# Optimization experiments

Hardware: AMD Instinct MI355X
Metric: run time of the kernel (lower is better)

Reference implementation:

```python
import jax, jax.numpy as jnp
import numpy as np

DIM = 768
NUM_HEADS = 12
HEAD_DIM = DIM // NUM_HEADS
SCALE = HEAD_DIM ** -0.5


def setup_inputs() -> dict:
    key = jax.random.key(0)
    ks = jax.random.split(key, 12)
    B, N, C, H = 8, 1024, DIM, NUM_HEADS
    s = 0.02
    return {
        'q_in': jax.random.normal(ks[0], (B, N, C), jnp.float32),
        'kv_in': jax.random.normal(ks[1], (B, N, C), jnp.float32),
        'Wq': jax.random.normal(ks[2], (C, C), jnp.float32) * s,
        'Wk': jax.random.normal(ks[3], (C, C), jnp.float32) * s,
        'Wv': jax.random.normal(ks[4], (C, C), jnp.float32) * s,
        'Wp': jax.random.normal(ks[5], (C, C), jnp.float32) * s,
        'bp': jnp.zeros((C,), jnp.float32),
        'W_dy2': jax.random.normal(ks[6], (H, C), jnp.float32) * s,  # lf gate linear (out=H)
        'b_dy2': jnp.zeros((H,), jnp.float32),
        'W_dy': jax.random.normal(ks[7], (H, C), jnp.float32) * s,   # hf gate linear
        'b_dy': jnp.zeros((H,), jnp.float32),
        'lf_gamma': jnp.full((C,), 1e-5, jnp.float32),
        'hf_gamma': jnp.full((C,), 1e-5, jnp.float32),
        'star_scale': jnp.ones((1,), jnp.float32),
        'star_bias': jnp.zeros((1,), jnp.float32),
    }


def reference(q_in, kv_in, Wq, Wk, Wv, Wp, bp, W_dy2, b_dy2, W_dy, b_dy,
              lf_gamma, hf_gamma, star_scale, star_bias):
    B, Nq, C = q_in.shape
    Nk = kv_in.shape[1]
    H, D = NUM_HEADS, HEAD_DIM

    # StarReLU on query tokens (ignore_cls_token = 0)
    dy_feat = star_scale * jnp.square(jax.nn.relu(q_in)) + star_bias  # (B,Nq,C)

    # low-freq dynamic gate: tanh(linear) per head, repeated over head_dim
    dy_lf = jnp.tanh(jnp.einsum('bnc,hc->bnh', dy_feat, W_dy2) + b_dy2)  # (B,Nq,H)
    dy_lf = jnp.repeat(dy_lf, D, axis=-1)  # (B,Nq,C)

    # high-freq dynamic gate: rational-of-softplus^2
    dy = jax.nn.softplus(jnp.einsum('bnc,hc->bnh', dy_feat, W_dy) + b_dy)
    dy2 = jnp.square(dy)
    dy_hf = 2.0 * dy2 / (dy2 + 0.3678)
    dy_hf = jnp.repeat(dy_hf, D, axis=-1)  # (B,Nq,C)

    # projections (torch Linear: y = x @ W.T), split heads
    q = jnp.einsum('bnc,dc->bnd', q_in, Wq).reshape(B, Nq, H, D).transpose(0, 2, 1, 3)
    k = jnp.einsum('bnc,dc->bnd', kv_in, Wk).reshape(B, Nk, H, D).transpose(0, 2, 1, 3)
    v = jnp.einsum('bnc,dc->bnd', kv_in, Wv).reshape(B, Nk, H, D).transpose(0, 2, 1, 3)

    attn = jnp.einsum('bhqd,bhkd->bhqk', q * SCALE, k)
    attn = jax.nn.softmax(attn, axis=-1)
    x_attn = jnp.einsum('bhqk,bhkd->bhqd', attn, v)
    x_attn = x_attn.transpose(0, 2, 1, 3).reshape(B, Nq, C)

    # Nk == Nq branch: per-token residual high-frequency component
    v_reshape = v.transpose(0, 2, 1, 3).reshape(B, Nk, C)
    v_hf = v_reshape - x_attn

    x_attn = x_attn + x_attn * dy_lf * lf_gamma
    x_attn = x_attn + dy_hf * v_hf * hf_gamma

    out = jnp.einsum('bnc,dc->bnd', x_attn, Wp) + bp
    return out
```

## Files before the change

### kernel.cpp

```cpp
#include <hip/hip_runtime.h>
#include <hip/hip_bf16.h>
#include <stdint.h>

typedef unsigned short u16;
typedef unsigned int u32;
typedef unsigned long long u64;
typedef __attribute__((ext_vector_type(8))) short short8;
typedef __attribute__((ext_vector_type(4))) float f32x4;

#define LOG2E 1.44269504f

static __device__ __forceinline__ u16 f2bf(float f) {
    u32 x = __float_as_uint(f);
    u32 r = (x + 0x7FFFu + ((x >> 16) & 1u)) >> 16;
    return (u16)r;
}
static __device__ __forceinline__ float bf2f(u16 u) {
    return __uint_as_float(((u32)u) << 16);
}
static __device__ __forceinline__ u32 pk2(float lo, float hi) {
    __hip_bfloat162 t = __float22bfloat162_rn(float2{lo, hi});
    union { __hip_bfloat162 b; u32 u; } cv;
    cv.b = t;
    return cv.u;
}
static __device__ __forceinline__ float fexp2(float x) {
#if __has_builtin(__builtin_amdgcn_exp2f)
    return __builtin_amdgcn_exp2f(x);
#else
    return exp2f(x);
#endif
}

static __device__ __forceinline__ void g2l16(const void* g, void* l) {
    __builtin_amdgcn_global_load_lds((const __attribute__((address_space(1))) void*)g,
                                     (__attribute__((address_space(3))) void*)l, 16, 0, 0);
}

__global__ __launch_bounds__(256) void k_cvt_all(
    const float* __restrict__ q_in, const float* __restrict__ kv_in,
    const float* __restrict__ Wq, const float* __restrict__ Wk,
    const float* __restrict__ Wv, const float* __restrict__ Wp,
    const float* __restrict__ Wdy2, const float* __restrict__ Wdy,
    u16* __restrict__ qbf, u16* __restrict__ kvbf, u16* __restrict__ Wqb,
    u16* __restrict__ Wkb, u16* __restrict__ Wvb, u16* __restrict__ Wpb,
    u16* __restrict__ wgb) {
    int i = blockIdx.x * 256 + threadIdx.x;
    const float* src;
    u16* dst;
    int so, dofs;
    if (i < 786432) { src = q_in; dst = qbf; so = i; dofs = i; }
    else if (i < 1572864) { src = kv_in; dst = kvbf; so = i - 786432; dofs = so; }
    else if (i < 1646592) { src = Wq; dst = Wqb; so = i - 1572864; dofs = so; }
    else if (i < 1720320) { src = Wk; dst = Wkb; so = i - 1646592; dofs = so; }
    else if (i < 1794048) { src = Wv; dst = Wvb; so = i - 1720320; dofs = so; }
    else if (i < 1867776) { src = Wp; dst = Wpb; so = i - 1794048; dofs = so; }
    else if (i < 1870080) {
        int e = i - 1867776;
        dst = wgb; dofs = e;
        if (e < 1152) { src = Wdy2; so = e; }
        else { src = Wdy; so = e - 1152; }
    } else return;
    const float4* p = (const float4*)src + (size_t)so * 2;
    float4 a = p[0], b = p[1];
    short8 o;
    o[0] = f2bf(a.x); o[1] = f2bf(a.y); o[2] = f2bf(a.z); o[3] = f2bf(a.w);
    o[4] = f2bf(b.x); o[5] = f2bf(b.y); o[6] = f2bf(b.z); o[7] = f2bf(b.w);
    *((short8*)dst + dofs) = o;
}

__global__ __launch_bounds__(64) void k_gates(
    const u16* __restrict__ qbf, const u16* __restrict__ wgb,
    const float* __restrict__ bdy2, const float* __restrict__ bdy,
    const float* __restrict__ star_s, const float* __restrict__ star_b,
    float* __restrict__ glf, float* __restrict__ ghf) {
    int lane = threadIdx.x;
    int g = lane >> 4, c = lane & 15;
    int row0 = blockIdx.x * 16;
    float ss = star_s[0], sb = star_b[0];
    f32x4 acc[2];
    acc[0] = (f32x4){0.f, 0.f, 0.f, 0.f};
    acc[1] = (f32x4){0.f, 0.f, 0.f, 0.f};
    for (int t = 0; t < 24; ++t) {
        int k0 = t * 32;
        short8 x8 = *(const short8*)(qbf + (size_t)(row0 + c) * 768 + k0 + g * 8);
        float f[8];
#pragma unroll
        for (int j = 0; j < 8; ++j) {
            float x = fmaxf(bf2f((u16)x8[j]), 0.f);
            f[j] = ss * x * x + sb;
        }
        union { u32 u[4]; short8 s8; } au;
#pragma unroll
        for (int j = 0; j < 4; ++j) au.u[j] = pk2(f[2 * j], f[2 * j + 1]);
        short8 b0 = *(const short8*)(wgb + (size_t)c * 768 + k0 + g * 8);
        short8 b1 = (short8){0, 0, 0, 0, 0, 0, 0, 0};
        if (c < 8)
            b1 = *(const short8*)(wgb + (size_t)(16 + c) * 768 + k0 + g * 8);
        acc[0] = __builtin_amdgcn_mfma_f32_16x16x32_bf16(au.s8, b0, acc[0], 0, 0, 0);
        acc[1] = __builtin_amdgcn_mfma_f32_16x16x32_bf16(au.s8, b1, acc[1], 0, 0, 0);
    }
#pragma unroll
    for (int n = 0; n < 2; ++n)
#pragma unroll
        for (int r = 0; r < 4; ++r) {
            int token = row0 + g * 4 + r;
            int o = n * 16 + c;
            float v = acc[n][r];
            if (o < 12) {
                glf[(size_t)token * 12 + o] = tanhf(v + bdy2[o]);
            } else if (o < 24) {
                float x = v + bdy[o - 12];
                float sp = (x > 15.f) ? x : log1pf(expf(x));
                float d2 = sp * sp;
                ghf[(size_t)token * 12 + (o - 12)] = 2.f * d2 / (d2 + 0.3678f);
            }
        }
}

__device__ __forceinline__ void gemm_core(const u16* __restrict__ A,
                                          const u16* __restrict__ W, u16* As,
                                          u16* Bs, int rowA0, int rowB0,
                                          int lane, int w, int wm, int wn,
                                          f32x4 acc[4][4]) {
    int g = lane >> 4, c = lane & 15;
#pragma unroll
    for (int m = 0; m < 4; ++m)
#pragma unroll
        for (int n = 0; n < 4; ++n) acc[m][n] = (f32x4){0.f, 0.f, 0.f, 0.f};

    auto stage = [&](int buf, int k0) {
#pragma unroll
        for (int j = 0; j < 2; ++j) {
            int L = w * 128 + j * 64 + lane;
            int p = L >> 3, s8 = L & 7;
            int t2 = s8 ^ (p & 7);
            int row = 2 * p + (t2 >> 2);
            int chunk = t2 & 3;
            size_t go = (size_t)row * 768 + k0 + chunk * 8;
            g2l16(A + (size_t)rowA0 * 768 + go, As + buf * 4096 + L * 8);
            g2l16(W + (size_t)rowB0 * 768 + go, Bs + buf * 4096 + L * 8);
        }
    };

    stage(0, 0);
    stage(1, 32);
    int cur = 0, nxt = 2;
    for (int t = 0; t < 24; ++t) {
        if (t < 23) asm volatile("s_waitcnt vmcnt(4)" ::: "memory");
        else        asm volatile("s_waitcnt vmcnt(0)" ::: "memory");
        __builtin_amdgcn_s_barrier();
        if (t < 22) stage(nxt, (t + 2) * 32);
        short8 a[4], b[4];
#pragma unroll
        for (int m = 0; m < 4; ++m) {
            int row = wm * 64 + m * 16 + c;
            int off = (row >> 1) * 64 +
                      ((((row & 1) << 2) | g) ^ ((row >> 1) & 7)) * 8;
            a[m] = *(const short8*)(As + cur * 4096 + off);
        }
#pragma unroll
        for (int n = 0; n < 4; ++n) {
            int row = wn * 64 + n * 16 + c;
            int off = (row >> 1) * 64 +
                      ((((row & 1) << 2) | g) ^ ((row >> 1) & 7)) * 8;
            b[n] = *(const short8*)(Bs + cur * 4096 + off);
        }
        __builtin_amdgcn_s_setprio(1);
#pragma unroll
        for (int m = 0; m < 4; ++m)
#pragma unroll
            for (int n = 0; n < 4; ++n)
                acc[m][n] = __builtin_amdgcn_mfma_f32_16x16x32_bf16(
                    a[m], b[n], acc[m][n], 0, 0, 0);
        __builtin_amdgcn_s_setprio(0);
        cur = (cur == 2) ? 0 : cur + 1;
        nxt = (nxt == 2) ? 0 : nxt + 1;
    }
}

static __device__ __forceinline__ int park_wb(int row, int col) {
    return row * 256 + ((col * 2) ^ (((row >> 2) & 3) << 5));
}
static __device__ __forceinline__ int park_rb(int srow, int sch) {
    return srow * 256 + ((sch * 16) ^ (((srow >> 2) & 3) << 5));
}

__global__ __launch_bounds__(256, 3) void k_gemm_qkv(
    const u16* __restrict__ qbf, const u16* __restrict__ kvbf,
    const u16* __restrict__ Wqb, const u16* __restrict__ Wkb,
    const u16* __restrict__ Wvb, u16* __restrict__ Qb, u16* __restrict__ Kb,
    u16* __restrict__ VTg, u16* __restrict__ vlin) {
    __shared__ __align__(16) u16 smem[24576];
    u16* As = smem;
    u16* Bs = smem + 12288;
    int bid = blockIdx.x;
    int logical = (bid & 7) * 144 + (bid >> 3);
    int panel = logical / 18, sub = logical % 18;
    int type = sub / 6, tn = sub % 6;
    int tid = threadIdx.x, lane = tid & 63, w = tid >> 6;
    int g = lane >> 4, c = lane & 15;
    int wm = w >> 1, wn = w & 1;
    int rowA0 = panel * 128, rowB0 = tn * 128;
    const u16* A = (type == 0) ? qbf : kvbf;
    const u16* W = (type == 0) ? Wqb : (type == 1) ? Wkb : Wvb;

    f32x4 acc[4][4];
    gemm_core(A, W, As, Bs, rowA0, rowB0, lane, w, wm, wn, acc);
    __syncthreads();

    if (type < 2) {
        u16* dst = (type == 0) ? Qb : Kb;
        const float scl = (type == 0) ? (0.125f * LOG2E) : 1.0f;
#pragma unroll
        for (int m = 0; m < 4; ++m)
#pragma unroll
            for (int n = 0; n < 4; ++n)
#pragma unroll
                for (int r = 0; r < 4; ++r) {
                    int row = wm * 64 + m * 16 + g * 4 + r;
                    int col = wn * 64 + n * 16 + c;
                    *(u16*)((char*)smem + park_wb(row, col)) =
                        f2bf(acc[m][n][r] * scl);
                }
        __syncthreads();
#pragma unroll
        for (int j = 0; j < 8; ++j) {
            int idx = j * 256 + tid;
            int srow = idx >> 4, sch = idx & 15;
            short8 v = *(const short8*)((char*)smem + park_rb(srow, sch));
            int token = rowA0 + srow;
            int col0 = rowB0 + sch * 8;
            int bb = token >> 10, nn = token & 1023, hh = col0 >> 6,
                dd = col0 & 63;
            *(short8*)(dst + ((size_t)(bb * 12 + hh) << 16) + (nn << 6) + dd) = v;
        }
    } else {
#pragma unroll
        for (int m = 0; m < 4; ++m)
#pragma unroll
            for (int n = 0; n < 4; ++n)
#pragma unroll
                for (int r = 0; r < 4; ++r) {
                    int row = wm * 64 + m * 16 + g * 4 + r;
                    int col = wn * 64 + n * 16 + c;
                    *(u16*)((char*)smem + park_wb(row, col)) = f2bf(acc[m][n][r]);
                }
        __syncthreads();
#pragma unroll
        for (int j = 0; j < 8; ++j) {
            int idx = j * 256 + tid;
            int srow = idx >> 4, sch = idx & 15;
            short8 v = *(const short8*)((char*)smem + park_rb(srow, sch));
            *(short8*)(vlin + (size_t)(rowA0 + srow) * 768 + rowB0 + sch * 8) = v;
        }
        __syncthreads();
#pragma unroll
        for (int m = 0; m < 4; ++m)
#pragma unroll
            for (int n = 0; n < 4; ++n)
#pragma unroll
                for (int r = 0; r < 4; ++r) {
                    int rl = wm * 64 + m * 16 + g * 4 + r;
                    int cl = wn * 64 + n * 16 + c;
                    smem[cl * 128 + rl] = f2bf(acc[m][n][r]);
                }
        __syncthreads();
        int bb = rowA0 >> 10, nn0 = rowA0 & 1023;
#pragma unroll
        for (int j = 0; j < 8; ++j) {
            int idx = j * 256 + tid;
            int rT = idx >> 4, cc = idx & 15;
            int dout = rowB0 + rT, hh = dout >> 6, dd = dout & 63;
            const u16* srow = smem + rT * 128 + cc * 8;
            size_t robase = ((size_t)(bb * 12 + hh) * 64 + dd) * 1024;
#pragma unroll
            for (int e2 = 0; e2 < 4; ++e2) {
                int n0 = nn0 + cc * 8 + 2 * e2;
                int t6 = n0 & 63;
                int pos = (((t6 >> 1) & 1) << 5) | (((t6 >> 2) & 3) << 3) |
                          (((t6 >> 4) & 3) << 1) | (t6 & 1);
                u32 val = (u32)srow[2 * e2] | ((u32)srow[2 * e2 + 1] << 16);
                *(u32*)(VTg + robase + (n0 & ~63) + pos) = val;
            }
        }
    }
}

__global__ __launch_bounds__(256, 3) void k_gemm_out(
    const u16* __restrict__ xf, const u16* __restrict__ Wpb,
    const float* __restrict__ bp, float* __restrict__ out) {
    __shared__ __align__(16) u16 smem[24576];
    u16* As = smem;
    u16* Bs = smem + 12288;
    int bid = blockIdx.x;
    int logical = (bid & 7) * 48 + (bid >> 3);
    int c48 = logical % 48;
    int tm = (logical / 48) * 8 + c48 / 6, tn = c48 % 6;
    int tid = threadIdx.x, lane = tid & 63, w = tid >> 6;
    int g = lane >> 4, c = lane & 15;
    int wm = w >> 1, wn = w & 1;
    int rowA0 = tm * 128, rowB0 = tn * 128;

    f32x4 acc[4][4];
    gemm_core(xf, Wpb, As, Bs, rowA0, rowB0, lane, w, wm, wn, acc);

    float bias[4];
#pragma unroll
    for (int n = 0; n < 4; ++n) bias[n] = bp[rowB0 + wn * 64 + n * 16 + c];

    char* F = (char*)smem;
#pragma unroll
    for (int p = 0; p < 2; ++p) {
        __syncthreads();
        if (wm == p) {
#pragma unroll
            for (int m = 0; m < 4; ++m)
#pragma unroll
                for (int n = 0; n < 4; ++n)
#pragma unroll
                    for (int r = 0; r < 4; ++r) {
                        int lrow = m * 16 + g * 4 + r;
                        int col = wn * 64 + n * 16 + c;
                        int byte = lrow * 512 +
                                   ((col * 4) ^ (((lrow >> 2) & 3) << 6));
                        *(float*)(F + byte) = acc[m][n][r] + bias[n];
                    }
        }
        __syncthreads();
#pragma unroll
        for (int j = 0; j < 8; ++j) {
            int idx = j * 256 + tid;
            int srow = idx >> 5, sch = idx & 31;
            int byte = srow * 512 + ((sch * 16) ^ (((srow >> 2) & 3) << 6));
            float4 v = *(const float4*)(F + byte);
            *(float4*)(out + (size_t)(rowA0 + p * 64 + srow) * 768 + rowB0 +
                       sch * 4) = v;
        }
    }
}

__global__ __launch_bounds__(256, 3) void k_attn(
    const u16* __restrict__ Qb, const u16* __restrict__ Kb,
    const u16* __restrict__ VTg, const u16* __restrict__ vlin,
    const float* __restrict__ glf, const float* __restrict__ ghf,
    const float* __restrict__ lfg, const float* __restrict__ hfg,
    u16* __restrict__ xfinal) {
    __shared__ __align__(16) u16 Ks[12288];
    __shared__ __align__(16) u16 Vs[12288];
    int b8 = blockIdx.x;
    int sw = (b8 & 7) * 96 + (b8 >> 3);
    int bh = sw >> 3, qblk = sw & 7;
    int bb = bh / 12, hh = bh % 12;
    int tid = threadIdx.x, lane = tid & 63, w = tid >> 6;
    int g = lane >> 4, c = lane & 15;
    const char* Kp = (const char*)(Kb + ((size_t)bh << 16));
    const char* Vp = (const char*)(VTg + ((size_t)bh << 16));
    const u16* Qp = Qb + ((size_t)bh << 16);
    int q0 = qblk * 128 + w * 32;

    short8 qf[2][2];
#pragma unroll
    for (int qb = 0; qb < 2; ++qb)
#pragma unroll
        for (int ks = 0; ks < 2; ++ks)
            qf[qb][ks] = *(const short8*)(Qp + (size_t)(q0 + qb * 16 + c) * 64 +
                                          ks * 32 + g * 8);

    f32x4 o[2][4];
#pragma unroll
    for (int qb = 0; qb < 2; ++qb)
#pragma unroll
        for (int n = 0; n < 4; ++n) o[qb][n] = (f32x4){0.f, 0.f, 0.f, 0.f};
    f32x4 o5[2];
    o5[0] = (f32x4){0.f, 0.f, 0.f, 0.f};
    o5[1] = (f32x4){0.f, 0.f, 0.f, 0.f};
    const short8 vones = (short8){(short)0x3F80, (short)0x3F80, (short)0x3F80,
                                  (short)0x3F80, (short)0x3F80, (short)0x3F80,
                                  (short)0x3F80, (short)0x3F80};

    int kgo[2], vgo[2], ldo[2];
#pragma unroll
    for (int h = 0; h < 2; ++h) {
        int idx = w * 64 + lane + h * 256;
        int row = idx >> 3;
        int colb = ((idx & 7) * 16) ^ ((row & 7) << 4);
        kgo[h] = row * 128 + colb;
        vgo[h] = row * 2048 + colb;
        ldo[h] = (w * 64 + h * 256) * 16;
    }

    auto stage = [&](int bi, int t) {
#pragma unroll
        for (int h = 0; h < 2; ++h) {
            g2l16(Kp + (size_t)t * 8192 + kgo[h], (char*)Ks + bi * 8192 + ldo[h]);
            g2l16(Vp + (size_t)t * 128 + vgo[h], (char*)Vs + bi * 8192 + ldo[h]);
        }
    };

    stage(0, 0);
    stage(1, 1);
    int cur = 0, nxt = 2;
    int cs = (c & 7) << 4;
    for (int t = 0; t < 16; ++t) {
        if (t < 15) asm volatile("s_waitcnt vmcnt(4)" ::: "memory");
        else        asm volatile("s_waitcnt vmcnt(0)" ::: "memory");
        __builtin_amdgcn_s_barrier();
        if (t < 14) stage(nxt, t + 2);
        const char* Kbase = (const char*)Ks + cur * 8192;
        const char* Vbase = (const char*)Vs + cur * 8192;
        short8 kf[4][2], vf[4][2];
#pragma unroll
        for (int m = 0; m < 4; ++m) {
            int rowb = (m * 16 + c) * 128;
#pragma unroll
            for (int ks = 0; ks < 2; ++ks)
                kf[m][ks] = *(const short8*)(Kbase + rowb +
                                             ((g * 16 + ks * 64) ^ cs));
        }
#pragma unroll
        for (int n = 0; n < 4; ++n) {
            int rowb = (n * 16 + c) * 128;
#pragma unroll
            for (int a = 0; a < 2; ++a)
                vf[n][a] = *(const short8*)(Vbase + rowb +
                                            ((a * 64 + g * 16) ^ cs));
        }
#pragma unroll
        for (int qb = 0; qb < 2; ++qb) {
            f32x4 s[4];
            __builtin_amdgcn_s_setprio(1);
#pragma unroll
            for (int m = 0; m < 4; ++m) {
                s[m] = __builtin_amdgcn_mfma_f32_16x16x32_bf16(
                    kf[m][0], qf[qb][0], (f32x4){0.f, 0.f, 0.f, 0.f}, 0, 0, 0);
                s[m] = __builtin_amdgcn_mfma_f32_16x16x32_bf16(
                    kf[m][1], qf[qb][1], s[m], 0, 0, 0);
            }
            __builtin_amdgcn_s_setprio(0);
            u32 P2[4][2];
#pragma unroll
            for (int m = 0; m < 4; ++m) {
#pragma unroll
                for (int r = 0; r < 4; ++r) s[m][r] = fexp2(s[m][r]);
                P2[m][0] = pk2(s[m][0], s[m][1]);
                P2[m][1] = pk2(s[m][2], s[m][3]);
            }
#pragma unroll
            for (int a = 0; a < 2; ++a) {
                union { u32 u[4]; short8 s8; } pu;
                pu.u[0] = P2[0][a]; pu.u[1] = P2[1][a];
                pu.u[2] = P2[2][a]; pu.u[3] = P2[3][a];
                __builtin_amdgcn_s_setprio(1);
#pragma unroll
                for (int n = 0; n < 4; ++n)
                    o[qb][n] = __builtin_amdgcn_mfma_f32_16x16x32_bf16(
                        pu.s8, vf[n][a], o[qb][n], 0, 0, 0);
                o5[qb] = __builtin_amdgcn_mfma_f32_16x16x32_bf16(
                    pu.s8, vones, o5[qb], 0, 0, 0);
                __builtin_amdgcn_s_setprio(0);
            }
        }
        cur = (cur == 2) ? 0 : cur + 1;
        nxt = (nxt == 2) ? 0 : nxt + 1;
    }
    __syncthreads();

    u16* X = &Ks[0];
#pragma unroll
    for (int qb = 0; qb < 2; ++qb) {
        float rl[4];
#pragma unroll
        for (int r = 0; r < 4; ++r) rl[r] = 1.0f / o5[qb][r];
#pragma unroll
        for (int n = 0; n < 4; ++n)
#pragma unroll
            for (int r = 0; r < 4; ++r) {
                int row = w * 32 + qb * 16 + 4 * g + r;
                int col = n * 16 + c;
                int byte = row * 128 + ((col * 2) ^ ((row & 3) << 4));
                *(u16*)((char*)X + byte) = f2bf(o[qb][n][r] * rl[r]);
            }
    }
    __syncthreads();
    {
        int row = tid >> 1, half = tid & 1;
        size_t token = (size_t)bb * 1024 + qblk * 128 + row;
        float alf = glf[token * 12 + hh];
        float ahf = ghf[token * 12 + hh];
        int dbase = hh * 64 + half * 32;
        const u16* vbase = vlin + token * 768 + dbase;
        u16* obase = xfinal + token * 768 + dbase;
#pragma unroll
        for (int j = 0; j < 4; ++j) {
            int phys = ((half * 4 + j) ^ (row & 3)) * 16;
            short8 xa8 = *(const short8*)((char*)X + row * 128 + phys);
            short8 vl8 = *(const short8*)(vbase + j * 8);
            float4 lg0 = *(const float4*)(lfg + dbase + j * 8);
            float4 lg1 = *(const float4*)(lfg + dbase + j * 8 + 4);
            float4 hg0 = *(const float4*)(hfg + dbase + j * 8);
            float4 hg1 = *(const float4*)(hfg + dbase + j * 8 + 4);
            float lg[8] = {lg0.x, lg0.y, lg0.z, lg0.w, lg1.x, lg1.y, lg1.z, lg1.w};
            float hg[8] = {hg0.x, hg0.y, hg0.z, hg0.w, hg1.x, hg1.y, hg1.z, hg1.w};
            short8 oo;
#pragma unroll
            for (int e = 0; e < 8; ++e) {
                float xa = bf2f((u16)xa8[e]);
                float v = bf2f((u16)vl8[e]);
                float val = xa + xa * alf * lg[e] + ahf * (v - xa) * hg[e];
                oo[e] = f2bf(val);
            }
            *(short8*)(obase + j * 8) = oo;
        }
    }
}

extern "C" void kernel_launch(void* const* d_in, const int* in_sizes, int n_in,
                              void* d_out, int out_size, void* d_ws,
                              size_t ws_size, hipStream_t stream) {
    const float* q_in = (const float*)d_in[0];
    const float* kv_in = (const float*)d_in[1];
    const float* Wq = (const float*)d_in[2];
    const float* Wk = (const float*)d_in[3];
    const float* Wv = (const float*)d_in[4];
    const float* Wp = (const float*)d_in[5];
    const float* bp = (const float*)d_in[6];
    const float* Wdy2 = (const float*)d_in[7];
    const float* bdy2 = (const float*)d_in[8];
    const float* Wdy = (const float*)d_in[9];
    const float* bdy = (const float*)d_in[10];
    const float* lfg = (const float*)d_in[11];
    const float* hfg = (const float*)d_in[12];
    const float* st_s = (const float*)d_in[13];
    const float* st_b = (const float*)d_in[14];
    float* out = (float*)d_out;

    char* ws = (char*)d_ws;
    const size_t MC2 = (size_t)8192 * 768 * 2;
    const size_t WB = (size_t)768 * 768 * 2;
    u16* qbf = (u16*)(ws);
    u16* kvbf = (u16*)(ws + MC2);
    u16* Wqb = (u16*)(ws + 2 * MC2);
    u16* Wkb = (u16*)(ws + 2 * MC2 + WB);
    u16* Wvb = (u16*)(ws + 2 * MC2 + 2 * WB);
    u16* Wpb = (u16*)(ws + 2 * MC2 + 3 * WB);
    u16* Qb = (u16*)(ws + 2 * MC2 + 4 * WB);
    u16* Kb = (u16*)(ws + 3 * MC2 + 4 * WB);
    u16* VTg = (u16*)(ws + 4 * MC2 + 4 * WB);
    u16* vlin = (u16*)(ws + 5 * MC2 + 4 * WB);
    float* glf = (float*)(ws + 6 * MC2 + 4 * WB);
    float* ghf = (float*)(ws + 6 * MC2 + 4 * WB + (size_t)8192 * 12 * 4);
    u16* wgb = (u16*)(ws + 6 * MC2 + 4 * WB + (size_t)8192 * 12 * 8);
    u16* xfinal = qbf;

    k_cvt_all<<<7305, 256, 0, stream>>>(q_in, kv_in, Wq, Wk, Wv, Wp, Wdy2,
                                        Wdy, qbf, kvbf, Wqb, Wkb, Wvb, Wpb,
                                        wgb);
    k_gates<<<512, 64, 0, stream>>>(qbf, wgb, bdy2, bdy, st_s, st_b, glf, ghf);
    k_gemm_qkv<<<1152, 256, 0, stream>>>(qbf, kvbf, Wqb, Wkb, Wvb, Qb, Kb,
                                         VTg, vlin);
    k_attn<<<768, 256, 0, stream>>>(Qb, Kb, VTg, vlin, glf, ghf, lfg, hfg,
                                    xfinal);
    k_gemm_out<<<384, 256, 0, stream>>>(xfinal, Wpb, bp, out);
}
```

Before: 133.7 us.

## Fuse activation fp32-to-bf16 conversion into QKV GEMM and drop attention LDS staging

Stops pre-converting q_in and kv_in to bf16 in a separate pass. The QKV GEMM now loads fp32 A tiles into registers and converts and writes them to LDS itself, and the gates kernel reads fp32 directly. This removes a full activation read and write pass over global memory. Separately, the attention kernel now reads K and V fragments straight from global memory instead of through triple-buffered LDS, freeing shared memory so occupancy can rise to 4 blocks per SM; this risks uncoalesced, redundant global loads and exposed latency.

Result: slower. 244.7 us (+83.0%).

```diff
diff --git a/kernel.cpp b/kernel.cpp
--- a/kernel.cpp
+++ b/kernel.cpp
@@ -37,26 +37,22 @@
                                      (__attribute__((address_space(3))) void*)l, 16, 0, 0);
 }
 
-__global__ __launch_bounds__(256) void k_cvt_all(
-    const float* __restrict__ q_in, const float* __restrict__ kv_in,
+__global__ __launch_bounds__(256) void k_cvt_w(
     const float* __restrict__ Wq, const float* __restrict__ Wk,
     const float* __restrict__ Wv, const float* __restrict__ Wp,
     const float* __restrict__ Wdy2, const float* __restrict__ Wdy,
-    u16* __restrict__ qbf, u16* __restrict__ kvbf, u16* __restrict__ Wqb,
-    u16* __restrict__ Wkb, u16* __restrict__ Wvb, u16* __restrict__ Wpb,
-    u16* __restrict__ wgb) {
+    u16* __restrict__ Wqb, u16* __restrict__ Wkb, u16* __restrict__ Wvb,
+    u16* __restrict__ Wpb, u16* __restrict__ wgb) {
     int i = blockIdx.x * 256 + threadIdx.x;
     const float* src;
     u16* dst;
     int so, dofs;
-    if (i < 786432) { src = q_in; dst = qbf; so = i; dofs = i; }
-    else if (i < 1572864) { src = kv_in; dst = kvbf; so = i - 786432; dofs = so; }
-    else if (i < 1646592) { src = Wq; dst = Wqb; so = i - 1572864; dofs = so; }
-    else if (i < 1720320) { src = Wk; dst = Wkb; so = i - 1646592; dofs = so; }
-    else if (i < 1794048) { src = Wv; dst = Wvb; so = i - 1720320; dofs = so; }
-    else if (i < 1867776) { src = Wp; dst = Wpb; so = i - 1794048; dofs = so; }
-    else if (i < 1870080) {
-        int e = i - 1867776;
+    if (i < 73728) { src = Wq; dst = Wqb; so = i; dofs = so; }
+    else if (i < 147456) { src = Wk; dst = Wkb; so = i - 73728; dofs = so; }
+    else if (i < 221184) { src = Wv; dst = Wvb; so = i - 147456; dofs = so; }
+    else if (i < 294912) { src = Wp; dst = Wpb; so = i - 221184; dofs = so; }
+    else if (i < 297216) {
+        int e = i - 294912;
         dst = wgb; dofs = e;
         if (e < 1152) { src = Wdy2; so = e; }
         else { src = Wdy; so = e - 1152; }
@@ -70,7 +66,7 @@
 }
 
 __global__ __launch_bounds__(64) void k_gates(
-    const u16* __restrict__ qbf, const u16* __restrict__ wgb,
+    const float* __restrict__ qin, const u16* __restrict__ wgb,
     const float* __restrict__ bdy2, const float* __restrict__ bdy,
     const float* __restrict__ star_s, const float* __restrict__ star_b,
     float* __restrict__ glf, float* __restrict__ ghf) {
@@ -83,11 +79,13 @@
     acc[1] = (f32x4){0.f, 0.f, 0.f, 0.f};
     for (int t = 0; t < 24; ++t) {
         int k0 = t * 32;
-        short8 x8 = *(const short8*)(qbf + (size_t)(row0 + c) * 768 + k0 + g * 8);
-        float f[8];
+        const float* qrow = qin + (size_t)(row0 + c) * 768 + k0 + g * 8;
+        float4 xa = *(const float4*)qrow;
+        float4 xb = *(const float4*)(qrow + 4);
+        float f[8] = {xa.x, xa.y, xa.z, xa.w, xb.x, xb.y, xb.z, xb.w};
 #pragma unroll
         for (int j = 0; j < 8; ++j) {
-            float x = fmaxf(bf2f((u16)x8[j]), 0.f);
+            float x = fmaxf(f[j], 0.f);
             f[j] = ss * x * x + sb;
         }
         union { u32 u[4]; short8 s8; } au;
@@ -118,67 +116,6 @@
         }
 }
 
-__device__ __forceinline__ void gemm_core(const u16* __restrict__ A,
-                                          const u16* __restrict__ W, u16* As,
-                                          u16* Bs, int rowA0, int rowB0,
-                                          int lane, int w, int wm, int wn,
-                                          f32x4 acc[4][4]) {
-    int g = lane >> 4, c = lane & 15;
-#pragma unroll
-    for (int m = 0; m < 4; ++m)
-#pragma unroll
-        for (int n = 0; n < 4; ++n) acc[m][n] = (f32x4){0.f, 0.f, 0.f, 0.f};
-
-    auto stage = [&](int buf, int k0) {
-#pragma unroll
-        for (int j = 0; j < 2; ++j) {
-            int L = w * 128 + j * 64 + lane;
-            int p = L >> 3, s8 = L & 7;
-            int t2 = s8 ^ (p & 7);
-            int row = 2 * p + (t2 >> 2);
-            int chunk = t2 & 3;
-            size_t go = (size_t)row * 768 + k0 + chunk * 8;
-            g2l16(A + (size_t)rowA0 * 768 + go, As + buf * 4096 + L * 8);
-            g2l16(W + (size_t)rowB0 * 768 + go, Bs + buf * 4096 + L * 8);
-        }
-    };
-
-    stage(0, 0);
-    stage(1, 32);
-    int cur = 0, nxt = 2;
-    for (int t = 0; t < 24; ++t) {
-        if (t < 23) asm volatile("s_waitcnt vmcnt(4)" ::: "memory");
-        else        asm volatile("s_waitcnt vmcnt(0)" ::: "memory");
-        __builtin_amdgcn_s_barrier();
-        if (t < 22) stage(nxt, (t + 2) * 32);
-        short8 a[4], b[4];
-#pragma unroll
-        for (int m = 0; m < 4; ++m) {
-            int row = wm * 64 + m * 16 + c;
-            int off = (row >> 1) * 64 +
-                      ((((row & 1) << 2) | g) ^ ((row >> 1) & 7)) * 8;
-            a[m] = *(const short8*)(As + cur * 4096 + off);
-        }
-#pragma unroll
-        for (int n = 0; n < 4; ++n) {
-            int row = wn * 64 + n * 16 + c;
-            int off = (row >> 1) * 64 +
-                      ((((row & 1) << 2) | g) ^ ((row >> 1) & 7)) * 8;
-            b[n] = *(const short8*)(Bs + cur * 4096 + off);
-        }
-        __builtin_amdgcn_s_setprio(1);
-#pragma unroll
-        for (int m = 0; m < 4; ++m)
-#pragma unroll
-            for (int n = 0; n < 4; ++n)
-                acc[m][n] = __builtin_amdgcn_mfma_f32_16x16x32_bf16(
-                    a[m], b[n], acc[m][n], 0, 0, 0);
-        __builtin_amdgcn_s_setprio(0);
-        cur = (cur == 2) ? 0 : cur + 1;
-        nxt = (nxt == 2) ? 0 : nxt + 1;
-    }
-}
-
 static __device__ __forceinline__ int park_wb(int row, int col) {
     return row * 256 + ((col * 2) ^ (((row >> 2) & 3) << 5));
 }
@@ -187,7 +124,7 @@
 }
 
 __global__ __launch_bounds__(256, 3) void k_gemm_qkv(
-    const u16* __restrict__ qbf, const u16* __restrict__ kvbf,
+    const float* __restrict__ qf32, const float* __restrict__ kvf32,
     const u16* __restrict__ Wqb, const u16* __restrict__ Wkb,
     const u16* __restrict__ Wvb, u16* __restrict__ Qb, u16* __restrict__ Kb,
     u16* __restrict__ VTg, u16* __restrict__ vlin) {
@@ -202,11 +139,94 @@
     int g = lane >> 4, c = lane & 15;
     int wm = w >> 1, wn = w & 1;
     int rowA0 = panel * 128, rowB0 = tn * 128;
-    const u16* A = (type == 0) ? qbf : kvbf;
+    const float* Af = (type == 0) ? qf32 : kvf32;
     const u16* W = (type == 0) ? Wqb : (type == 1) ? Wkb : Wvb;
 
+    int Lrow[2], Lch[2], Llds[2];
+#pragma unroll
+    for (int j = 0; j < 2; ++j) {
+        int L = w * 128 + j * 64 + lane;
+        int p = L >> 3, s8 = L & 7;
+        int t2 = s8 ^ (p & 7);
+        Lrow[j] = 2 * p + (t2 >> 2);
+        Lch[j] = t2 & 3;
+        Llds[j] = L * 8;
+    }
+    float4 ar[2][2];
+    auto loadA = [&](int k0) {
+#pragma unroll
+        for (int j = 0; j < 2; ++j) {
+            const float* s = Af + (size_t)(rowA0 + Lrow[j]) * 768 + k0 + Lch[j] * 8;
+            ar[j][0] = *(const float4*)s;
+            ar[j][1] = *(const float4*)(s + 4);
+        }
+    };
+    auto writeA = [&](int buf) {
+#pragma unroll
+        for (int j = 0; j < 2; ++j) {
+            union { u32 u[4]; short8 s8; } pv;
+            pv.u[0] = pk2(ar[j][0].x, ar[j][0].y);
+            pv.u[1] = pk2(ar[j][0].z, ar[j][0].w);
+            pv.u[2] = pk2(ar[j][1].x, ar[j][1].y);
+            pv.u[3] = pk2(ar[j][1].z, ar[j][1].w);
+            *(short8*)(As + buf * 4096 + Llds[j]) = pv.s8;
+        }
+    };
+    auto loadB = [&](int buf, int k0) {
+#pragma unroll
+        for (int j = 0; j < 2; ++j) {
+            size_t go = (size_t)(rowB0 + Lrow[j]) * 768 + k0 + Lch[j] * 8;
+            g2l16(W + go, Bs + buf * 4096 + (w * 128 + j * 64) * 8);
+        }
+    };
+
     f32x4 acc[4][4];
-    gemm_core(A, W, As, Bs, rowA0, rowB0, lane, w, wm, wn, acc);
+#pragma unroll
+    for (int m = 0; m < 4; ++m)
+#pragma unroll
+        for (int n = 0; n < 4; ++n) acc[m][n] = (f32x4){0.f, 0.f, 0.f, 0.f};
+
+    loadA(0);
+    loadB(0, 0);
+    asm volatile("s_waitcnt vmcnt(2)" ::: "memory");
+    writeA(0);
+    loadA(32);
+    loadB(1, 32);
+
+    for (int t = 0; t < 24; ++t) {
+        if (t < 23) asm volatile("s_waitcnt vmcnt(2) lgkmcnt(0)" ::: "memory");
+        else        asm volatile("s_waitcnt vmcnt(0) lgkmcnt(0)" ::: "memory");
+        __builtin_amdgcn_s_barrier();
+        if (t < 23) writeA((t + 1) % 3);
+        if (t < 22) {
+            loadA((t + 2) * 32);
+            loadB((t + 2) % 3, (t + 2) * 32);
+        }
+        int cur = t % 3;
+        short8 a[4], b[4];
+#pragma unroll
+        for (int m = 0; m < 4; ++m) {
+            int row = wm * 64 + m * 16 + c;
+            int off = (row >> 1) * 64 +
+                      ((((row & 1) << 2) | g) ^ ((row >> 1) & 7)) * 8;
+            a[m] = *(const short8*)(As + cur * 4096 + off);
+        }
+#pragma unroll
+        for (int n = 0; n < 4; ++n) {
+            int row = wn * 64 + n * 16 + c;
+            int off = (row >> 1) * 64 +
+                      ((((row & 1) << 2) | g) ^ ((row >> 1) & 7)) * 8;
+            b[n] = *(const short8*)(Bs + cur * 4096 + off);
+        }
+        __builtin_amdgcn_s_setprio(1);
+#pragma unroll
+        for (int m = 0; m < 4; ++m)
+#pragma unroll
+            for (int n = 0; n < 4; ++n)
+                acc[m][n] = __builtin_amdgcn_mfma_f32_16x16x32_bf16(
+                    a[m], b[n], acc[m][n], 0, 0, 0);
+        __builtin_amdgcn_s_setprio(0);
+    }
     __syncthreads();
 
     if (type < 2) {
@@ -284,6 +304,68 @@
                 *(u32*)(VTg + robase + (n0 & ~63) + pos) = val;
             }
         }
+    }
+}
+
+__device__ __forceinline__ void gemm_core_bf16(const u16* __restrict__ A,
+                                               const u16* __restrict__ W,
+                                               u16* As, u16* Bs, int rowA0,
+                                               int rowB0, int lane, int w,
+                                               int wm, int wn,
+                                               f32x4 acc[4][4]) {
+    int g = lane >> 4, c = lane & 15;
+#pragma unroll
+    for (int m = 0; m < 4; ++m)
+#pragma unroll
+        for (int n = 0; n < 4; ++n) acc[m][n] = (f32x4){0.f, 0.f, 0.f, 0.f};
+
+    auto stage = [&](int buf, int k0) {
+#pragma unroll
+        for (int j = 0; j < 2; ++j) {
+            int L = w * 128 + j * 64 + lane;
+            int p = L >> 3, s8 = L & 7;
+            int t2 = s8 ^ (p & 7);
+            int row = 2 * p + (t2 >> 2);
+            int chunk = t2 & 3;
+            size_t go = (size_t)row * 768 + k0 + chunk * 8;
+            g2l16(A + (size_t)rowA0 * 768 + go, As + buf * 4096 + (w * 128 + j * 64) * 8);
+            g2l16(W + (size_t)rowB0 * 768 + go, Bs + buf * 4096 + (w * 128 + j * 64) * 8);
+        }
+    };
+
+    stage(0, 0);
+    stage(1, 32);
+    int cur = 0, nxt = 2;
+    for (int t = 0; t < 24; ++t) {
+        if (t < 23) asm volatile("s_waitcnt vmcnt(4)" ::: "memory");
+        else        asm volatile("s_waitcnt vmcnt(0)" ::: "memory");
+        __builtin_amdgcn_s_barrier();
+        if (t < 22) stage(nxt, (t + 2) * 32);
+        short8 a[4], b[4];
+#pragma unroll
+        for (int m = 0; m < 4; ++m) {
+            int row = wm * 64 + m * 16 + c;
+            int off = (row >> 1) * 64 +
+                      ((((row & 1) << 2) | g) ^ ((row >> 1) & 7)) * 8;
+            a[m] = *(const short8*)(As + cur * 4096 + off);
+        }
+#pragma unroll
+        for (int n = 0; n < 4; ++n) {
+            int row = wn * 64 + n * 16 + c;
+            int off = (row >> 1) * 64 +
+                      ((((row & 1) << 2) | g) ^ ((row >> 1) & 7)) * 8;
+            b[n] = *(const short8*)(Bs + cur * 4096 + off);
+        }
+        __builtin_amdgcn_s_setprio(1);
+#pragma unroll
+        for (int m = 0; m < 4; ++m)
+#pragma unroll
+            for (int n = 0; n < 4; ++n)
+                acc[m][n] = __builtin_amdgcn_mfma_f32_16x16x32_bf16(
+                    a[m], b[n], acc[m][n], 0, 0, 0);
+        __builtin_amdgcn_s_setprio(0);
+        cur = (cur == 2) ? 0 : cur + 1;
+        nxt = (nxt == 2) ? 0 : nxt + 1;
     }
 }
 
@@ -303,7 +385,7 @@
     int rowA0 = tm * 128, rowB0 = tn * 128;
 
     f32x4 acc[4][4];
-    gemm_core(xf, Wpb, As, Bs, rowA0, rowB0, lane, w, wm, wn, acc);
+    gemm_core_bf16(xf, Wpb, As, Bs, rowA0, rowB0, lane, w, wm, wn, acc);
 
     float bias[4];
 #pragma unroll
@@ -340,14 +422,13 @@
     }
 }
 
-__global__ __launch_bounds__(256, 3) void k_attn(
+__global__ __launch_bounds__(256, 4) void k_attn(
     const u16* __restrict__ Qb, const u16* __restrict__ Kb,
     const u16* __restrict__ VTg, const u16* __restrict__ vlin,
     const float* __restrict__ glf, const float* __restrict__ ghf,
     const float* __restrict__ lfg, const float* __restrict__ hfg,
     u16* __restrict__ xfinal) {
-    __shared__ __align__(16) u16 Ks[12288];
-    __shared__ __align__(16) u16 Vs[12288];
+    __shared__ __align__(16) u16 X[8192];
     int b8 = blockIdx.x;
     int sw = (b8 & 7) * 96 + (b8 >> 3);
     int bh = sw >> 3, qblk = sw & 7;
@@ -379,53 +460,22 @@
                                   (short)0x3F80, (short)0x3F80, (short)0x3F80,
                                   (short)0x3F80, (short)0x3F80};
 
-    int kgo[2], vgo[2], ldo[2];
-#pragma unroll
-    for (int h = 0; h < 2; ++h) {
-        int idx = w * 64 + lane + h * 256;
-        int row = idx >> 3;
-        int colb = ((idx & 7) * 16) ^ ((row & 7) << 4);
-        kgo[h] = row * 128 + colb;
-        vgo[h] = row * 2048 + colb;
-        ldo[h] = (w * 64 + h * 256) * 16;
-    }
-
-    auto stage = [&](int bi, int t) {
-#pragma unroll
-        for (int h = 0; h < 2; ++h) {
-            g2l16(Kp + (size_t)t * 8192 + kgo[h], (char*)Ks + bi * 8192 + ldo[h]);
-            g2l16(Vp + (size_t)t * 128 + vgo[h], (char*)Vs + bi * 8192 + ldo[h]);
-        }
-    };
-
-    stage(0, 0);
-    stage(1, 1);
-    int cur = 0, nxt = 2;
-    int cs = (c & 7) << 4;
     for (int t = 0; t < 16; ++t) {
-        if (t < 15) asm volatile("s_waitcnt vmcnt(4)" ::: "memory");
-        else        asm volatile("s_waitcnt vmcnt(0)" ::: "memory");
-        __builtin_amdgcn_s_barrier();
-        if (t < 14) stage(nxt, t + 2);
-        const char* Kbase = (const char*)Ks + cur * 8192;
-        const char* Vbase = (const char*)Vs + cur * 8192;
+        const char* Ktile = Kp + (size_t)t * 8192;
+        const char* Vtile = Vp + (size_t)t * 128;
         short8 kf[4][2], vf[4][2];
 #pragma unroll
-        for (int m = 0; m < 4; ++m) {
-            int rowb = (m * 16 + c) * 128;
+        for (int m = 0; m < 4; ++m)
 #pragma unroll
             for (int ks = 0; ks < 2; ++ks)
-                kf[m][ks] = *(const short8*)(Kbase + rowb +
-                                             ((g * 16 + ks * 64) ^ cs));
-        }
-#pragma unroll
-        for (int n = 0; n < 4; ++n) {
-            int rowb = (n * 16 + c) * 128;
+                kf[m][ks] = *(const short8*)(Ktile + (m * 16 + c) * 128 +
+                                             ks * 64 + g * 16);
+#pragma unroll
+        for (int n = 0; n < 4; ++n)
 #pragma unroll
             for (int a = 0; a < 2; ++a)
-                vf[n][a] = *(const short8*)(Vbase + rowb +
-                                            ((a * 64 + g * 16) ^ cs));
-        }
+                vf[n][a] = *(const short8*)(Vtile + (size_t)(n * 16 + c) * 2048 +
+                                            a * 64 + g * 16);
 #pragma unroll
         for (int qb = 0; qb < 2; ++qb) {
             f32x4 s[4];
@@ -461,12 +511,8 @@
                 __builtin_amdgcn_s_setprio(0);
             }
         }
-        cur = (cur == 2) ? 0 : cur + 1;
-        nxt = (nxt == 2) ? 0 : nxt + 1;
-    }
-    __syncthreads();
-
-    u16* X = &Ks[0];
+    }
+
 #pragma unroll
     for (int qb = 0; qb < 2; ++qb) {
         float rl[4];
@@ -538,8 +584,7 @@
     char* ws = (char*)d_ws;
     const size_t MC2 = (size_t)8192 * 768 * 2;
     const size_t WB = (size_t)768 * 768 * 2;
-    u16* qbf = (u16*)(ws);
-    u16* kvbf = (u16*)(ws + MC2);
+    u16* xfinal = (u16*)(ws);
     u16* Wqb = (u16*)(ws + 2 * MC2);
     u16* Wkb = (u16*)(ws + 2 * MC2 + WB);
     u16* Wvb = (u16*)(ws + 2 * MC2 + 2 * WB);
@@ -551,13 +596,12 @@
     float* glf = (float*)(ws + 6 * MC2 + 4 * WB);
     float* ghf = (float*)(ws + 6 * MC2 + 4 * WB + (size_t)8192 * 12 * 4);
     u16* wgb = (u16*)(ws + 6 * MC2 + 4 * WB + (size_t)8192 * 12 * 8);
-    u16* xfinal = qbf;
-
-    k_cvt_all<<<7305, 256, 0, stream>>>(q_in, kv_in, Wq, Wk, Wv, Wp, Wdy2,
-                                        Wdy, qbf, kvbf, Wqb, Wkb, Wvb, Wpb,
-                                        wgb);
-    k_gates<<<512, 64, 0, stream>>>(qbf, wgb, bdy2, bdy, st_s, st_b, glf, ghf);
-    k_gemm_qkv<<<1152, 256, 0, stream>>>(qbf, kvbf, Wqb, Wkb, Wvb, Qb, Kb,
+
+    k_cvt_w<<<1161, 256, 0, stream>>>(Wq, Wk, Wv, Wp, Wdy2, Wdy, Wqb, Wkb,
+                                      Wvb, Wpb, wgb);
+    k_gates<<<512, 64, 0, stream>>>(q_in, wgb, bdy2, bdy, st_s, st_b, glf,
+                                    ghf);
+    k_gemm_qkv<<<1152, 256, 0, stream>>>(q_in, kv_in, Wqb, Wkb, Wvb, Qb, Kb,
                                          VTg, vlin);
     k_attn<<<768, 256, 0, stream>>>(Qb, Kb, VTg, vlin, glf, ghf, lfg, hfg,
                                     xfinal);
```
